# Performance work log

Hardware: AMD Instinct MI355X
Metric: run time of the kernel (lower is better)

The kernel has to match this reference:

```python
import jax, jax.numpy as jnp
import numpy as np

N = 50000       # nodes
E = 800000      # edges
C_IN = 64
C_OUT = 64
G = 128         # graphs in the batch
EPS = 1e-5      # BatchNorm eps


def setup_inputs() -> dict:
    key = jax.random.key(0)
    ks = jax.random.split(key, 9)
    x = jax.random.normal(ks[0], (N, C_IN), jnp.float32)
    edge_index = jax.random.randint(ks[1], (2, E), 0, N, dtype=jnp.int32)
    edge_weight = jax.random.uniform(ks[2], (E,), jnp.float32)
    batch = jnp.sort(jax.random.randint(ks[3], (N,), 0, G, dtype=jnp.int32))
    # SGConv linear params
    W = jax.random.normal(ks[4], (C_OUT, C_IN), jnp.float32) / np.sqrt(C_IN)
    b = 0.01 * jax.random.normal(ks[5], (C_OUT,), jnp.float32)
    # PReLU per-channel slope (torch init 0.25; perturb to exercise math)
    a = 0.25 + 0.01 * jax.random.normal(ks[6], (C_OUT,), jnp.float32)
    # BatchNorm affine params
    gamma = 1.0 + 0.1 * jax.random.normal(ks[7], (C_OUT,), jnp.float32)
    beta = 0.1 * jax.random.normal(ks[8], (C_OUT,), jnp.float32)
    return {"x": x, "edge_index": edge_index, "edge_weight": edge_weight,
            "batch": batch, "W": W, "b": b, "a": a, "gamma": gamma, "beta": beta}


def reference(x, edge_index, edge_weight, batch, W, b, a, gamma, beta):
    n = x.shape[0]
    loop = jnp.arange(n)
    # gcn_norm with self-loops (SGConv default)
    row = jnp.concatenate([edge_index[0], loop])      # source
    col = jnp.concatenate([edge_index[1], loop])      # target
    w = jnp.concatenate([edge_weight, jnp.ones((n,), x.dtype)])
    deg = jax.ops.segment_sum(w, col, num_segments=n)
    dinv = jnp.where(deg > 0, jax.lax.rsqrt(jnp.where(deg > 0, deg, 1.0)), 0.0)
    norm = dinv[row] * w * dinv[col]
    # K=2 hops of A_hat @ h, then linear
    h = x
    for _ in range(2):
        h = jax.ops.segment_sum(norm[:, None] * h[row], col, num_segments=n)
    h = h @ W.T + b
    # PReLU (per-channel)
    h = jnp.where(h >= 0, h, a * h)
    # BatchNorm1d, training-mode forward (batch stats, biased var)
    mu = h.mean(axis=0)
    var = jnp.mean((h - mu) ** 2, axis=0)
    h = (h - mu) * jax.lax.rsqrt(var + EPS) * gamma + beta
    # Global mean + max pooling per graph -> [G, 2*C_OUT]
    cnt = jax.ops.segment_sum(jnp.ones((n,), h.dtype), batch, num_segments=G)
    mean_p = jax.ops.segment_sum(h, batch, num_segments=G) / jnp.maximum(cnt, 1.0)[:, None]
    max_p = jax.ops.segment_max(h, batch, num_segments=G)
    return jnp.concatenate([mean_p, max_p], axis=1)
```

## Files before the change

kernel.cpp:

```cpp
#include <hip/hip_runtime.h>
#include <hip/hip_bf16.h>
#include <math.h>

#define NN 50000
#define NE 800000
#define CC 64
#define GG 128
#define KP 8
#define BINS ((NN + 255) / 256)
#define CAPB 4608
#define EPB 2048
#define GA ((NE + EPB - 1) / EPB)

typedef __hip_bfloat16 bf16;

__device__ inline unsigned short f2b(float f) {
    bf16 h = __float2bfloat16(f);
    return *reinterpret_cast<unsigned short*>(&h);
}
__device__ inline float blo(unsigned u) { return __uint_as_float(u << 16); }
__device__ inline float bhi(unsigned u) { return __uint_as_float(u & 0xffff0000u); }

__global__ void k_prep(int* bin_cnt, float* stats) {
    int t = threadIdx.x;
    if (t < BINS) bin_cnt[t] = 0;
    if (t < 2 * CC) stats[t] = 0.0f;
}

__global__ __launch_bounds__(256) void k_binA(const int* __restrict__ ei,
                                              const float* __restrict__ w,
                                              int* __restrict__ bin_cnt,
                                              int2* __restrict__ binbuf) {
    __shared__ int hist[BINS], base[BINS], rank[BINS];
    __shared__ int cstg[EPB];
    int t = threadIdx.x;
    for (int b = t; b < BINS; b += 256) { hist[b] = 0; rank[b] = 0; }
    __syncthreads();
    int e0 = blockIdx.x * EPB;
    for (int i = t; i < EPB; i += 256) {
        int e = e0 + i;
        if (e < NE) {
            int c = ei[NE + e];
            cstg[i] = c;
            atomicAdd(&hist[c >> 8], 1);
        }
    }
    __syncthreads();
    for (int b = t; b < BINS; b += 256)
        if (hist[b] > 0) base[b] = atomicAdd(&bin_cnt[b], hist[b]);
    __syncthreads();
    for (int i = t; i < EPB; i += 256) {
        int e = e0 + i;
        if (e >= NE) continue;
        int r = ei[e], c = cstg[i], b = c >> 8;
        int pos = base[b] + atomicAdd(&rank[b], 1);
        if (pos < CAPB)
            binbuf[(size_t)b * CAPB + pos] = make_int2(r | ((c & 255) << 16),
                                                       __float_as_int(w[e]));
    }
}

__global__ __launch_bounds__(256) void k_csr(const int* __restrict__ bin_cnt,
                                             int2* __restrict__ binbuf,
                                             float* __restrict__ dinv,
                                             int* __restrict__ rps,
                                             int* __restrict__ rcnt) {
    __shared__ int2 ed[CAPB];
    __shared__ int hist[256], off[256], rank[256];
    __shared__ float degf[256];
    int g = blockIdx.x, t = threadIdx.x;
    int cnt = min(bin_cnt[g], CAPB);
    int2* bp = binbuf + (size_t)g * CAPB;
    hist[t] = 0; rank[t] = 0; degf[t] = 1.0f;
    __syncthreads();
    for (int e = t; e < cnt; e += 256) {
        int2 r = bp[e];
        ed[e] = r;
        int low = r.x >> 16;
        atomicAdd(&hist[low], 1);
        atomicAdd(&degf[low], __int_as_float(r.y));
    }
    __syncthreads();
    int v = hist[t];
    off[t] = v;
    __syncthreads();
    for (int o = 1; o < 256; o <<= 1) {
        int x = (t >= o) ? off[t - o] : 0;
        __syncthreads();
        off[t] += x;
        __syncthreads();
    }
    int node = g * 256 + t;
    if (node < NN) {
        dinv[node] = rsqrtf(degf[t]);
        rps[node] = g * CAPB + (off[t] - v);
        rcnt[node] = v;
    }
    for (int e = t; e < cnt; e += 256) {
        int2 r = ed[e];
        int low = r.x >> 16;
        int pos = (off[low] - hist[low]) + atomicAdd(&rank[low], 1);
        bp[pos] = make_int2(r.x & 0xffff, r.y);
    }
}

__global__ __launch_bounds__(256) void k_linfold(const float* __restrict__ x,
                                                 const float* __restrict__ W,
                                                 const float* __restrict__ dinv,
                                                 const int* __restrict__ rps,
                                                 const int* __restrict__ rcnt,
                                                 const int2* __restrict__ binbuf,
                                                 unsigned* __restrict__ csrc,
                                                 bf16* __restrict__ y) {
    __shared__ float Ws[CC * 65];
    __shared__ float hs[4][CC];
    int tid = threadIdx.x, wv = tid >> 6, j = tid & 63;
    for (int t = tid; t < CC * CC; t += 256)
        Ws[(t >> 6) * 65 + (t & 63)] = W[t];
    int node = blockIdx.x * 4 + wv;
    hs[wv][j] = (node < NN) ? x[node * CC + j] : 0.0f;
    __syncthreads();
    if (node >= NN) return;
    float acc = 0.0f;
    const float* hr = hs[wv];
#pragma unroll
    for (int k = 0; k < CC; k++) acc += hr[k] * Ws[j * 65 + k];
    y[node * CC + j] = __float2bfloat16(acc);
    float dn = dinv[node];
    int s = rps[node], n = rcnt[node];
    for (int p = j; p < n; p += 64) {
        int2 rec = binbuf[s + p];
        float nw = dinv[rec.x] * __int_as_float(rec.y) * dn;
        csrc[s + p] = (unsigned)rec.x | ((unsigned)f2b(nw) << 16);
    }
}

__global__ __launch_bounds__(256) void k_hop8(const bf16* __restrict__ in,
                                              const float* __restrict__ dinv,
                                              const int* __restrict__ rps,
                                              const int* __restrict__ rcnt,
                                              const unsigned* __restrict__ csrc,
                                              bf16* __restrict__ out) {
    int node = blockIdx.x * 4 + (threadIdx.x >> 6);
    if (node >= NN) return;
    int lane = threadIdx.x & 63;
    int o = lane >> 3;
    int lc = lane & 7;
    float dn = dinv[node];
    float a0 = 0, a1 = 0, a2 = 0, a3 = 0, a4 = 0, a5 = 0, a6 = 0, a7 = 0;
    if (o == 0) {
        uint4 v = *reinterpret_cast<const uint4*>(&in[node * CC + 8 * lc]);
        float d2 = dn * dn;
        a0 = d2 * blo(v.x); a1 = d2 * bhi(v.x);
        a2 = d2 * blo(v.y); a3 = d2 * bhi(v.y);
        a4 = d2 * blo(v.z); a5 = d2 * bhi(v.z);
        a6 = d2 * blo(v.w); a7 = d2 * bhi(v.w);
    }
    int s = rps[node], n = rcnt[node];
    const unsigned* cp = csrc + s;
    int p = 0;
#pragma unroll 2
    for (; p + 8 <= n; p += 8) {
        unsigned rec = cp[p + o];
        float nw = bhi(rec);
        int src = rec & 0xffff;
        uint4 v = *reinterpret_cast<const uint4*>(&in[src * CC + 8 * lc]);
        a0 = fmaf(nw, blo(v.x), a0); a1 = fmaf(nw, bhi(v.x), a1);
        a2 = fmaf(nw, blo(v.y), a2); a3 = fmaf(nw, bhi(v.y), a3);
        a4 = fmaf(nw, blo(v.z), a4); a5 = fmaf(nw, bhi(v.z), a5);
        a6 = fmaf(nw, blo(v.w), a6); a7 = fmaf(nw, bhi(v.w), a7);
    }
    if (p < n && o < n - p) {
        unsigned rec = cp[p + o];
        float nw = bhi(rec);
        int src = rec & 0xffff;
        uint4 v = *reinterpret_cast<const uint4*>(&in[src * CC + 8 * lc]);
        a0 = fmaf(nw, blo(v.x), a0); a1 = fmaf(nw, bhi(v.x), a1);
        a2 = fmaf(nw, blo(v.y), a2); a3 = fmaf(nw, bhi(v.y), a3);
        a4 = fmaf(nw, blo(v.z), a4); a5 = fmaf(nw, bhi(v.z), a5);
        a6 = fmaf(nw, blo(v.w), a6); a7 = fmaf(nw, bhi(v.w), a7);
    }
#pragma unroll
    for (int d = 8; d < 64; d <<= 1) {
        a0 += __shfl_xor(a0, d, 64); a1 += __shfl_xor(a1, d, 64);
        a2 += __shfl_xor(a2, d, 64); a3 += __shfl_xor(a3, d, 64);
        a4 += __shfl_xor(a4, d, 64); a5 += __shfl_xor(a5, d, 64);
        a6 += __shfl_xor(a6, d, 64); a7 += __shfl_xor(a7, d, 64);
    }
    if (o == 0) {
        uint4 ov;
        ov.x = (unsigned)f2b(a0) | ((unsigned)f2b(a1) << 16);
        ov.y = (unsigned)f2b(a2) | ((unsigned)f2b(a3) << 16);
        ov.z = (unsigned)f2b(a4) | ((unsigned)f2b(a5) << 16);
        ov.w = (unsigned)f2b(a6) | ((unsigned)f2b(a7) << 16);
        *reinterpret_cast<uint4*>(&out[node * CC + 8 * lc]) = ov;
    }
}

__device__ inline int lbound(const int* __restrict__ batch, int g) {
    int lo = 0, hi = NN;
    while (lo < hi) {
        int mid = (lo + hi) >> 1;
        if (batch[mid] < g) lo = mid + 1; else hi = mid;
    }
    return lo;
}

__global__ __launch_bounds__(256) void k_poolstat2(const bf16* __restrict__ h,
                                                   const float* __restrict__ bvec,
                                                   const float* __restrict__ a,
                                                   const int* __restrict__ batch,
                                                   float* __restrict__ psum,
                                                   float* __restrict__ psq,
                                                   float* __restrict__ pmax,
                                                   float* __restrict__ pmin,
                                                   int* __restrict__ gcnt) {
    __shared__ float r0[4][CC], r1[4][CC], r2[4][CC], r3[4][CC];
    __shared__ int sse[2];
    int g = blockIdx.x >> 3, k = blockIdx.x & (KP - 1);
    int tid = threadIdx.x, w = tid >> 6, j = tid & 63;
    if (tid == 0) sse[0] = lbound(batch, g);
    if (tid == 1) sse[1] = lbound(batch, g + 1);
    __syncthreads();
    int s = sse[0], e = sse[1], n = e - s;
    if (tid == 0 && k == 0) gcnt[g] = n;
    int c0 = s + ((n * k) >> 3), c1 = s + ((n * (k + 1)) >> 3);
    float bs = bvec[j], as = a[j];
    float sum = 0.0f, sq = 0.0f, mx = -__builtin_inff(), mn = __builtin_inff();
    for (int i = c0 + w; i < c1; i += 4) {
        float v = __bfloat162float(h[i * CC + j]) + bs;
        v = v >= 0.0f ? v : as * v;
        sum += v;
        sq += v * v;
        mx = fmaxf(mx, v);
        mn = fminf(mn, v);
    }
    r0[w][j] = sum; r1[w][j] = sq; r2[w][j] = mx; r3[w][j] = mn;
    __syncthreads();
    if (w == 0) {
        int o = (k * GG + g) * CC + j;
        psum[o] = r0[0][j] + r0[1][j] + r0[2][j] + r0[3][j];
        psq[o]  = r1[0][j] + r1[1][j] + r1[2][j] + r1[3][j];
        pmax[o] = fmaxf(fmaxf(r2[0][j], r2[1][j]), fmaxf(r2[2][j], r2[3][j]));
        pmin[o] = fminf(fminf(r3[0][j], r3[1][j]), fminf(r3[2][j], r3[3][j]));
    }
}

__global__ __launch_bounds__(256) void k_red(const float* __restrict__ psum,
                                             const float* __restrict__ psq,
                                             const float* __restrict__ pmax,
                                             const float* __restrict__ pmin,
                                             float* __restrict__ gsum,
                                             float* __restrict__ gmax,
                                             float* __restrict__ gmin,
                                             float* __restrict__ stats) {
    __shared__ float r0[4][CC], r1[4][CC];
    int tid = threadIdx.x, w = tid >> 6, j = tid & 63;
    int g = blockIdx.x * 4 + w;
    float gs = 0.0f, gq = 0.0f, mx = -__builtin_inff(), mn = __builtin_inff();
#pragma unroll
    for (int k = 0; k < KP; k++) {
        int o = (k * GG + g) * CC + j;
        gs += psum[o];
        gq += psq[o];
        mx = fmaxf(mx, pmax[o]);
        mn = fminf(mn, pmin[o]);
    }
    gsum[g * CC + j] = gs;
    gmax[g * CC + j] = mx;
    gmin[g * CC + j] = mn;
    r0[w][j] = gs; r1[w][j] = gq;
    __syncthreads();
    if (w == 0) {
        atomicAdd(&stats[j], r0[0][j] + r0[1][j] + r0[2][j] + r0[3][j]);
        atomicAdd(&stats[CC + j], r1[0][j] + r1[1][j] + r1[2][j] + r1[3][j]);
    }
}

__global__ void k_final(const float* __restrict__ stats,
                        const float* __restrict__ gamma,
                        const float* __restrict__ beta,
                        const int* __restrict__ gcnt,
                        const float* __restrict__ gsum,
                        const float* __restrict__ gmax,
                        const float* __restrict__ gmin,
                        float* __restrict__ out) {
    int t = blockIdx.x * 256 + threadIdx.x;
    if (t >= GG * CC) return;
    int g = t >> 6, j = t & 63;
    float mean = stats[j] * (1.0f / NN);
    float var = stats[CC + j] * (1.0f / NN) - mean * mean;
    float sc = gamma[j] * rsqrtf(var + 1e-5f);
    float sh = beta[j] - mean * sc;
    int n = gcnt[g];
    if (n > 0) {
        out[g * 2 * CC + j] = sc * (gsum[t] / (float)n) + sh;
        out[g * 2 * CC + CC + j] = (sc >= 0.0f) ? sc * gmax[t] + sh
                                                : sc * gmin[t] + sh;
    } else {
        out[g * 2 * CC + j] = 0.0f;
        out[g * 2 * CC + CC + j] = -__builtin_inff();
    }
}

extern "C" void kernel_launch(void* const* d_in, const int* in_sizes, int n_in,
                              void* d_out, int out_size, void* d_ws, size_t ws_size,
                              hipStream_t stream) {
    const float* x = (const float*)d_in[0];
    const int* ei = (const int*)d_in[1];
    const float* ew = (const float*)d_in[2];
    const int* batch = (const int*)d_in[3];
    const float* W = (const float*)d_in[4];
    const float* b = (const float*)d_in[5];
    const float* a = (const float*)d_in[6];
    const float* gamma = (const float*)d_in[7];
    const float* beta = (const float*)d_in[8];
    float* out = (float*)d_out;

    float* ws = (float*)d_ws;
    float* dinv = ws;
    int* rps = (int*)(ws + 50048);
    int* rcnt = (int*)(ws + 2 * 50048);
    int* bin_cnt = (int*)(ws + 3 * 50048);
    float* stats = ws + 3 * 50048 + 256;
    int* gcnt = (int*)(stats + 256);
    float* gsum = (float*)(gcnt + 256);
    float* gmax = gsum + GG * CC;
    float* gmin = gmax + GG * CC;
    float* psum = gmin + GG * CC;
    float* psq = psum + KP * GG * CC;
    float* pmax = psq + KP * GG * CC;
    float* pmin = pmax + KP * GG * CC;
    int2* binbuf = (int2*)(pmin + KP * GG * CC);
    unsigned* csrc = (unsigned*)(binbuf + (size_t)BINS * CAPB);
    bf16* y = (bf16*)(csrc + (size_t)BINS * CAPB);
    bf16* h1 = y + (size_t)NN * CC;
    bf16* h2 = h1 + (size_t)NN * CC;

    dim3 blk(256);
    int gH = (NN + 3) / 4;

    k_prep<<<1, blk, 0, stream>>>(bin_cnt, stats);
    k_binA<<<GA, blk, 0, stream>>>(ei, ew, bin_cnt, binbuf);
    k_csr<<<BINS, blk, 0, stream>>>(bin_cnt, binbuf, dinv, rps, rcnt);
    k_linfold<<<gH, blk, 0, stream>>>(x, W, dinv, rps, rcnt, binbuf, csrc, y);

    k_hop8<<<gH, blk, 0, stream>>>(y, dinv, rps, rcnt, csrc, h1);
    k_hop8<<<gH, blk, 0, stream>>>(h1, dinv, rps, rcnt, csrc, h2);

    k_poolstat2<<<GG * KP, blk, 0, stream>>>(h2, b, a, batch, psum, psq, pmax,
                                             pmin, gcnt);
    k_red<<<GG / 4, blk, 0, stream>>>(psum, psq, pmax, pmin, gsum, gmax, gmin, stats);
    k_final<<<(GG * CC + 255) / 256, blk, 0, stream>>>(stats, gamma, beta, gcnt,
                                                       gsum, gmax, gmin, out);
}
```

Baseline: 131.4 us.

## Fuse edge-weight normalization into first hop, split linear kernel, retune partitions

The per-edge normalization and packing of CSR records moves out of the linear kernel and into the first propagation hop, which computes the weight, writes the packed record for the second hop, and uses it right away. The linear kernel becomes a plain matmul with no dependence on the CSR build. The hop loops drop the separate tail iteration in favour of a per-lane guard. Pooling partitions per graph double and edges per binning block double, trading more parallelism in pooling for fewer binning blocks, while the first hop now carries extra dinv gathers and stores.

Result: slower. 150.3 us (+14.4%).

```diff
diff --git a/kernel.cpp b/kernel.cpp
--- a/kernel.cpp
+++ b/kernel.cpp
@@ -6,10 +6,10 @@
 #define NE 800000
 #define CC 64
 #define GG 128
-#define KP 8
+#define KP 16
 #define BINS ((NN + 255) / 256)
 #define CAPB 4608
-#define EPB 2048
+#define EPB 4096
 #define GA ((NE + EPB - 1) / EPB)
 
 typedef __hip_bfloat16 bf16;
@@ -104,14 +104,9 @@
     }
 }
 
-__global__ __launch_bounds__(256) void k_linfold(const float* __restrict__ x,
-                                                 const float* __restrict__ W,
-                                                 const float* __restrict__ dinv,
-                                                 const int* __restrict__ rps,
-                                                 const int* __restrict__ rcnt,
-                                                 const int2* __restrict__ binbuf,
-                                                 unsigned* __restrict__ csrc,
-                                                 bf16* __restrict__ y) {
+__global__ __launch_bounds__(256) void k_lin(const float* __restrict__ x,
+                                             const float* __restrict__ W,
+                                             bf16* __restrict__ y) {
     __shared__ float Ws[CC * 65];
     __shared__ float hs[4][CC];
     int tid = threadIdx.x, wv = tid >> 6, j = tid & 63;
@@ -126,12 +121,63 @@
 #pragma unroll
     for (int k = 0; k < CC; k++) acc += hr[k] * Ws[j * 65 + k];
     y[node * CC + j] = __float2bfloat16(acc);
+}
+
+__global__ __launch_bounds__(256) void k_hop8f(const bf16* __restrict__ in,
+                                               const float* __restrict__ dinv,
+                                               const int* __restrict__ rps,
+                                               const int* __restrict__ rcnt,
+                                               const int2* __restrict__ binbuf,
+                                               unsigned* __restrict__ csrc,
+                                               bf16* __restrict__ out) {
+    int node = blockIdx.x * 4 + (threadIdx.x >> 6);
+    if (node >= NN) return;
+    int lane = threadIdx.x & 63;
+    int o = lane >> 3;
+    int lc = lane & 7;
     float dn = dinv[node];
+    float a0 = 0, a1 = 0, a2 = 0, a3 = 0, a4 = 0, a5 = 0, a6 = 0, a7 = 0;
+    if (o == 0) {
+        uint4 v = *reinterpret_cast<const uint4*>(&in[node * CC + 8 * lc]);
+        float d2 = dn * dn;
+        a0 = d2 * blo(v.x); a1 = d2 * bhi(v.x);
+        a2 = d2 * blo(v.y); a3 = d2 * bhi(v.y);
+        a4 = d2 * blo(v.z); a5 = d2 * bhi(v.z);
+        a6 = d2 * blo(v.w); a7 = d2 * bhi(v.w);
+    }
     int s = rps[node], n = rcnt[node];
-    for (int p = j; p < n; p += 64) {
-        int2 rec = binbuf[s + p];
-        float nw = dinv[rec.x] * __int_as_float(rec.y) * dn;
-        csrc[s + p] = (unsigned)rec.x | ((unsigned)f2b(nw) << 16);
+    const int2* bp = binbuf + s;
+    unsigned* cw = csrc + s;
+#pragma unroll 2
+    for (int p = 0; p < n; p += 8) {
+        if (o < n - p) {
+            int2 rec = bp[p + o];
+            int src = rec.x;
+            float nwf = dinv[src] * __int_as_float(rec.y) * dn;
+            unsigned nwb = (unsigned)f2b(nwf);
+            if (lc == 0) cw[p + o] = (unsigned)src | (nwb << 16);
+            float nw = __uint_as_float(nwb << 16);
+            uint4 v = *reinterpret_cast<const uint4*>(&in[src * CC + 8 * lc]);
+            a0 = fmaf(nw, blo(v.x), a0); a1 = fmaf(nw, bhi(v.x), a1);
+            a2 = fmaf(nw, blo(v.y), a2); a3 = fmaf(nw, bhi(v.y), a3);
+            a4 = fmaf(nw, blo(v.z), a4); a5 = fmaf(nw, bhi(v.z), a5);
+            a6 = fmaf(nw, blo(v.w), a6); a7 = fmaf(nw, bhi(v.w), a7);
+        }
+    }
+#pragma unroll
+    for (int d = 8; d < 64; d <<= 1) {
+        a0 += __shfl_xor(a0, d, 64); a1 += __shfl_xor(a1, d, 64);
+        a2 += __shfl_xor(a2, d, 64); a3 += __shfl_xor(a3, d, 64);
+        a4 += __shfl_xor(a4, d, 64); a5 += __shfl_xor(a5, d, 64);
+        a6 += __shfl_xor(a6, d, 64); a7 += __shfl_xor(a7, d, 64);
+    }
+    if (o == 0) {
+        uint4 ov;
+        ov.x = (unsigned)f2b(a0) | ((unsigned)f2b(a1) << 16);
+        ov.y = (unsigned)f2b(a2) | ((unsigned)f2b(a3) << 16);
+        ov.z = (unsigned)f2b(a4) | ((unsigned)f2b(a5) << 16);
+        ov.w = (unsigned)f2b(a6) | ((unsigned)f2b(a7) << 16);
+        *reinterpret_cast<uint4*>(&out[node * CC + 8 * lc]) = ov;
     }
 }
 
@@ -158,27 +204,18 @@
     }
     int s = rps[node], n = rcnt[node];
     const unsigned* cp = csrc + s;
-    int p = 0;
 #pragma unroll 2
-    for (; p + 8 <= n; p += 8) {
-        unsigned rec = cp[p + o];
-        float nw = bhi(rec);
-        int src = rec & 0xffff;
-        uint4 v = *reinterpret_cast<const uint4*>(&in[src * CC + 8 * lc]);
-        a0 = fmaf(nw, blo(v.x), a0); a1 = fmaf(nw, bhi(v.x), a1);
-        a2 = fmaf(nw, blo(v.y), a2); a3 = fmaf(nw, bhi(v.y), a3);
-        a4 = fmaf(nw, blo(v.z), a4); a5 = fmaf(nw, bhi(v.z), a5);
-        a6 = fmaf(nw, blo(v.w), a6); a7 = fmaf(nw, bhi(v.w), a7);
-    }
-    if (p < n && o < n - p) {
-        unsigned rec = cp[p + o];
-        float nw = bhi(rec);
-        int src = rec & 0xffff;
-        uint4 v = *reinterpret_cast<const uint4*>(&in[src * CC + 8 * lc]);
-        a0 = fmaf(nw, blo(v.x), a0); a1 = fmaf(nw, bhi(v.x), a1);
-        a2 = fmaf(nw, blo(v.y), a2); a3 = fmaf(nw, bhi(v.y), a3);
-        a4 = fmaf(nw, blo(v.z), a4); a5 = fmaf(nw, bhi(v.z), a5);
-        a6 = fmaf(nw, blo(v.w), a6); a7 = fmaf(nw, bhi(v.w), a7);
+    for (int p = 0; p < n; p += 8) {
+        if (o < n - p) {
+            unsigned rec = cp[p + o];
+            float nw = bhi(rec);
+            int src = rec & 0xffff;
+            uint4 v = *reinterpret_cast<const uint4*>(&in[src * CC + 8 * lc]);
+            a0 = fmaf(nw, blo(v.x), a0); a1 = fmaf(nw, bhi(v.x), a1);
+            a2 = fmaf(nw, blo(v.y), a2); a3 = fmaf(nw, bhi(v.y), a3);
+            a4 = fmaf(nw, blo(v.z), a4); a5 = fmaf(nw, bhi(v.z), a5);
+            a6 = fmaf(nw, blo(v.w), a6); a7 = fmaf(nw, bhi(v.w), a7);
+        }
     }
 #pragma unroll
     for (int d = 8; d < 64; d <<= 1) {
@@ -217,14 +254,14 @@
                                                    int* __restrict__ gcnt) {
     __shared__ float r0[4][CC], r1[4][CC], r2[4][CC], r3[4][CC];
     __shared__ int sse[2];
-    int g = blockIdx.x >> 3, k = blockIdx.x & (KP - 1);
+    int g = blockIdx.x >> 4, k = blockIdx.x & (KP - 1);
     int tid = threadIdx.x, w = tid >> 6, j = tid & 63;
     if (tid == 0) sse[0] = lbound(batch, g);
     if (tid == 1) sse[1] = lbound(batch, g + 1);
     __syncthreads();
     int s = sse[0], e = sse[1], n = e - s;
     if (tid == 0 && k == 0) gcnt[g] = n;
-    int c0 = s + ((n * k) >> 3), c1 = s + ((n * (k + 1)) >> 3);
+    int c0 = s + ((n * k) >> 4), c1 = s + ((n * (k + 1)) >> 4);
     float bs = bvec[j], as = a[j];
     float sum = 0.0f, sq = 0.0f, mx = -__builtin_inff(), mn = __builtin_inff();
     for (int i = c0 + w; i < c1; i += 4) {
@@ -343,9 +380,9 @@
     k_prep<<<1, blk, 0, stream>>>(bin_cnt, stats);
     k_binA<<<GA, blk, 0, stream>>>(ei, ew, bin_cnt, binbuf);
     k_csr<<<BINS, blk, 0, stream>>>(bin_cnt, binbuf, dinv, rps, rcnt);
-    k_linfold<<<gH, blk, 0, stream>>>(x, W, dinv, rps, rcnt, binbuf, csrc, y);
-
-    k_hop8<<<gH, blk, 0, stream>>>(y, dinv, rps, rcnt, csrc, h1);
+    k_lin<<<gH, blk, 0, stream>>>(x, W, y);
+
+    k_hop8f<<<gH, blk, 0, stream>>>(y, dinv, rps, rcnt, binbuf, csrc, h1);
     k_hop8<<<gH, blk, 0, stream>>>(h1, dinv, rps, rcnt, csrc, h2);
 
     k_poolstat2<<<GG * KP, blk, 0, stream>>>(h2, b, a, batch, psum, psq, pmax,
```
